# Performance work log

Measured on AMD Instinct MI355X. Metric: run time of the kernel, lower is better.

Reference implementation:

```python
import jax, jax.numpy as jnp
import numpy as np

WINDOW_SIZES = (8, 16)
NUM_HEADS = 4
EPS_LN = 1e-5
EPS_Z = 1e-6


def _unfold(x, ws, st):
    # torch nn.Unfold -> [B*L, ws*ws, C] with L blocks row-major over (nh, nw)
    B, C, H, W = x.shape
    nh = (H - ws) // st + 1
    nw = (W - ws) // st + 1
    ih = (jnp.arange(nh) * st)[:, None] + jnp.arange(ws)[None, :]  # [nh, ws]
    iw = (jnp.arange(nw) * st)[:, None] + jnp.arange(ws)[None, :]  # [nw, ws]
    p = x[:, :, ih][:, :, :, :, iw]            # [B,C,nh,ws,nw,ws]
    p = p.transpose(0, 2, 4, 3, 5, 1)          # [B,nh,nw,ws,ws,C]
    return p.reshape(B * nh * nw, ws * ws, C)


def _fold(win, ws, st, H, W):
    # torch nn.Fold: scatter-add overlapping patches back to [B,C,H,W]
    B_, N, C = win.shape
    nh = (H - ws) // st + 1
    nw = (W - ws) // st + 1
    B = B_ // (nh * nw)
    ih = (jnp.arange(nh) * st)[:, None] + jnp.arange(ws)[None, :]
    iw = (jnp.arange(nw) * st)[:, None] + jnp.arange(ws)[None, :]
    p = win.reshape(B, nh, nw, ws, ws, C).transpose(0, 5, 1, 3, 2, 4)  # [B,C,nh,ws,nw,ws]
    out = jnp.zeros((B, C, H, W), win.dtype)
    return out.at[:, :, ih[:, :, None, None], iw[None, None, :, :]].add(p)


def _ln(x, g, b):
    m = jnp.mean(x, -1, keepdims=True)
    v = jnp.var(x, -1, keepdims=True)
    return (x - m) * jax.lax.rsqrt(v + EPS_LN) * g + b


def _forward(high_stage, low_stage, conv_w, conv_b, ln_g, ln_b,
             wq, bq, wk, bk, wv, bv, wo, bo, window_weights, alpha):
    # 1x1 conv: high_channel -> base_channel
    hs = jnp.einsum('bchw,oc->bohw', high_stage, conv_w) + conv_b[None, :, None, None]
    B, C, Hl, Wl = low_stage.shape
    H, W = hs.shape[2], hs.shape[3]
    s = Hl // H                      # Scale_spatial
    h = NUM_HEADS
    dh = C // h
    folded = []
    for i, ws in enumerate(WINDOW_SIZES):
        wsq = s * ws
        # queries from low stage (overlapping scaled windows)
        qw = _ln(_unfold(low_stage, wsq, wsq // 2), ln_g, ln_b)   # [B_,Nq,C]
        B_, Nq, _ = qw.shape
        q = (qw @ wq.T + bq).reshape(B_, Nq, h, dh).transpose(0, 2, 1, 3)
        q = jax.nn.elu(q) + 1.0                                    # [B_,h,Nq,dh]
        # keys/values from high stage windows
        fw = _ln(_unfold(hs, ws, ws // 2), ln_g, ln_b)             # [B_,Nk,C]
        Nk = fw.shape[1]
        k = (fw @ wk.T + bk).reshape(B_, Nk, h, dh).transpose(0, 2, 1, 3)
        k = jax.nn.elu(k) + 1.0
        v = (fw @ wv.T + bv).reshape(B_, Nk, h, dh).transpose(0, 2, 1, 3)
        # kernelized linear attention
        kmean = jnp.mean(k, axis=2)                                # [B_,h,dh]
        z = 1.0 / (jnp.einsum('bhnd,bhd->bhn', q, kmean) + EPS_Z)[..., None]
        kv = jnp.einsum('bhnd,bhne->bhde', k, v) / ws              # (k^T/sqrt(ws)) @ (v/sqrt(ws))
        out = jnp.einsum('bhnd,bhde->bhne', q, kv) * z * window_weights[i]
        out = out.transpose(0, 2, 1, 3).reshape(B_, Nq, C) @ wo.T + bo
        folded.append(_fold(out, wsq, wsq // 2, Hl, Wl))
    out = sum(folded) / len(folded)
    final = alpha[0] * out + (1.0 - alpha[0]) * low_stage
    return out, final


def setup_inputs():
    key = jax.random.key(0)
    ks = jax.random.split(key, 8)
    B, Ch, Cb, Hh, Wh, s = 8, 256, 128, 64, 64, 2
    sc = 0.02
    d = {}
    d['high_stage'] = jax.random.normal(ks[0], (B, Ch, Hh, Wh), jnp.float32)
    d['low_stage'] = jax.random.normal(ks[1], (B, Cb, Hh * s, Wh * s), jnp.float32)
    d['conv_w'] = jax.random.normal(ks[2], (Cb, Ch), jnp.float32) * sc
    d['conv_b'] = jnp.zeros((Cb,), jnp.float32)
    d['ln_g'] = jnp.ones((Cb,), jnp.float32)
    d['ln_b'] = jnp.zeros((Cb,), jnp.float32)
    d['wq'] = jax.random.normal(ks[3], (Cb, Cb), jnp.float32) * sc
    d['bq'] = jnp.zeros((Cb,), jnp.float32)
    d['wk'] = jax.random.normal(ks[4], (Cb, Cb), jnp.float32) * sc
    d['bk'] = jnp.zeros((Cb,), jnp.float32)
    d['wv'] = jax.random.normal(ks[5], (Cb, Cb), jnp.float32) * sc
    d['bv'] = jnp.zeros((Cb,), jnp.float32)
    d['wo'] = jax.random.normal(ks[6], (Cb, Cb), jnp.float32) * sc
    d['bo'] = jnp.zeros((Cb,), jnp.float32)
    d['window_weights'] = jnp.ones((len(WINDOW_SIZES),), jnp.float32)
    d['alpha'] = jnp.ones((1,), jnp.float32)
    return d


def reference(high_stage, low_stage, conv_w, conv_b, ln_g, ln_b,
              wq, bq, wk, bk, wv, bv, wo, bo, window_weights, alpha):
    out, final = _forward(high_stage, low_stage, conv_w, conv_b, ln_g, ln_b,
                          wq, bq, wk, bk, wv, bv, wo, bo, window_weights, alpha)
    return (out, final)
```

## Files before the change

### kernel.cpp

```cpp
#include <hip/hip_runtime.h>

#define NB 8
#define CH 256
#define CB 128
#define HSW 64
#define HSP (HSW*HSW)
#define LW 128
#define LP (LW*LW)

typedef __attribute__((ext_vector_type(8))) short bf16x8;
typedef __attribute__((ext_vector_type(4))) float f32x4;

__device__ inline ushort f2bf(float x) {
  uint u = __float_as_uint(x);
  uint r = (u + 0x7fffu + ((u >> 16) & 1u)) >> 16;
  return (ushort)r;
}
__device__ inline float bf2f(uint u) { return __uint_as_float(u << 16); }

__device__ inline bf16x8 ldg8(const ushort* p) {
  uint2 lo = *(const uint2*)p;
  uint2 hi = *(const uint2*)(p + 4);
  uint4 u = make_uint4(lo.x, lo.y, hi.x, hi.y);
  return *(bf16x8*)&u;
}

static constexpr size_t S_KVU = (size_t)NB*HSP*CB;

static constexpr size_t OFF_KCM   = 0;
static constexpr size_t OFF_VCM   = OFF_KCM + S_KVU/2;
static constexpr size_t OFF_KM8   = OFF_VCM + S_KVU/2;
static constexpr size_t OFF_KV8T  = OFF_KM8 + (size_t)1800*128;
static constexpr size_t OFF_KM16  = OFF_KV8T + (size_t)1800*4096/2;
static constexpr size_t OFF_KV16T = OFF_KM16 + (size_t)392*128;
static constexpr size_t OFF_WQB   = OFF_KV16T + (size_t)392*4096/2;
static constexpr size_t OFF_WKB   = OFF_WQB + 8192;
static constexpr size_t OFF_WVB   = OFF_WKB + 8192;
static constexpr size_t OFF_WOB   = OFF_WVB + 8192;
static constexpr size_t OFF_CWB   = OFF_WOB + 8192;

__global__ __launch_bounds__(256)
void k_castw(const float* __restrict__ s0, const float* __restrict__ s1,
             const float* __restrict__ s2, const float* __restrict__ s3,
             const float* __restrict__ s4,
             ushort* __restrict__ d0, ushort* __restrict__ d1,
             ushort* __restrict__ d2, ushort* __restrict__ d3,
             ushort* __restrict__ d4) {
  int y = blockIdx.y;
  const float* s; ushort* d; int n;
  if (y == 0)      { s = s0; d = d0; n = 16384; }
  else if (y == 1) { s = s1; d = d1; n = 16384; }
  else if (y == 2) { s = s2; d = d2; n = 16384; }
  else if (y == 3) { s = s3; d = d3; n = 16384; }
  else             { s = s4; d = d4; n = 32768; }
  int i = (blockIdx.x * 256 + threadIdx.x) * 8;
  if (i >= n) return;
  float4 a = *(const float4*)(s + i);
  float4 b = *(const float4*)(s + i + 4);
  bf16x8 pk;
  pk[0]=(short)f2bf(a.x); pk[1]=(short)f2bf(a.y); pk[2]=(short)f2bf(a.z); pk[3]=(short)f2bf(a.w);
  pk[4]=(short)f2bf(b.x); pk[5]=(short)f2bf(b.y); pk[6]=(short)f2bf(b.z); pk[7]=(short)f2bf(b.w);
  *(bf16x8*)(d + i) = pk;
}

#define A1S 264
__global__ __launch_bounds__(256)
void k_convkv(const float* __restrict__ high, const ushort* __restrict__ cwb,
              const float* __restrict__ cb, const float* __restrict__ lng,
              const float* __restrict__ lnb,
              const ushort* __restrict__ wkb, const float* __restrict__ bk,
              const ushort* __restrict__ wvb, const float* __restrict__ bv,
              ushort* __restrict__ kcm, ushort* __restrict__ vcm) {
  __shared__ __align__(16) ushort As1[64*A1S];
  __shared__ __align__(16) ushort As2[64*136];
  __shared__ float red[512];
  __shared__ float stat_m[64], stat_r[64];
  int t = threadIdx.x;
  size_t pixbase = (size_t)blockIdx.x * 64;
  int b = blockIdx.x >> 6;
  int prel = (int)(pixbase & (HSP - 1));
  const float* xb = high + (size_t)b*CH*HSP + prel;

  {
    int p = t & 63;
    int cp = (t >> 6) * 2;
    #pragma unroll 4
    for (int pass = 0; pass < 32; ++pass) {
      int c = pass*8 + cp;
      float v0 = xb[(size_t)c*HSP + p];
      float v1 = xb[(size_t)(c+1)*HSP + p];
      uint pk = (uint)f2bf(v0) | ((uint)f2bf(v1) << 16);
      *(uint*)&As1[p*A1S + c] = pk;
    }
  }
  __syncthreads();

  int l = t & 63, h = t >> 6;
  int lr = l & 15, lg = l >> 4;
  int n0 = h * 32;

  f32x4 acc[4][2];
  #pragma unroll
  for (int mt = 0; mt < 4; ++mt)
    #pragma unroll
    for (int nt = 0; nt < 2; ++nt) acc[mt][nt] = (f32x4){0.f,0.f,0.f,0.f};
  #pragma unroll
  for (int k0 = 0; k0 < 256; k0 += 32) {
    bf16x8 a[4], bw[2];
    #pragma unroll
    for (int mt = 0; mt < 4; ++mt)
      a[mt] = *(bf16x8*)&As1[(mt*16+lr)*A1S + k0 + lg*8];
    #pragma unroll
    for (int nt = 0; nt < 2; ++nt)
      bw[nt] = *(const bf16x8*)(cwb + (size_t)(n0 + nt*16 + lr)*256 + k0 + lg*8);
    #pragma unroll
    for (int mt = 0; mt < 4; ++mt)
      #pragma unroll
      for (int nt = 0; nt < 2; ++nt)
        acc[mt][nt] = __builtin_amdgcn_mfma_f32_16x16x32_bf16(a[mt], bw[nt], acc[mt][nt], 0,0,0);
  }
  {
    float cb0 = cb[n0 + lr], cb1 = cb[n0 + 16 + lr];
    #pragma unroll
    for (int mt = 0; mt < 4; ++mt)
      #pragma unroll
      for (int r = 0; r < 4; ++r) { acc[mt][0][r] += cb0; acc[mt][1][r] += cb1; }
  }
  #pragma unroll
  for (int mt = 0; mt < 4; ++mt)
    #pragma unroll
    for (int r = 0; r < 4; ++r) {
      float a0 = acc[mt][0][r], a1 = acc[mt][1][r];
      float s = a0 + a1, ss = a0*a0 + a1*a1;
      #pragma unroll
      for (int off = 1; off < 16; off <<= 1) {
        s  += __shfl_xor(s, off, 64);
        ss += __shfl_xor(ss, off, 64);
      }
      if (lr == 0) {
        int p = mt*16 + lg*4 + r;
        red[h*64 + p] = s;
        red[256 + h*64 + p] = ss;
      }
    }
  __syncthreads();
  if (t < 64) {
    float s  = red[t] + red[64+t] + red[128+t] + red[192+t];
    float ss = red[256+t] + red[320+t] + red[384+t] + red[448+t];
    float m = s * (1.f/128.f);
    float var = ss * (1.f/128.f) - m*m;
    stat_m[t] = m;
    stat_r[t] = rsqrtf(fmaxf(var, 0.f) + 1e-5f);
  }
  __syncthreads();
  {
    float g0 = lng[n0+lr], b0 = lnb[n0+lr];
    float g1 = lng[n0+16+lr], b1 = lnb[n0+16+lr];
    #pragma unroll
    for (int mt = 0; mt < 4; ++mt)
      #pragma unroll
      for (int r = 0; r < 4; ++r) {
        int p = mt*16 + lg*4 + r;
        float m = stat_m[p], rr = stat_r[p];
        As2[p*136 + n0 + lr]      = f2bf((acc[mt][0][r] - m)*rr*g0 + b0);
        As2[p*136 + n0 + 16 + lr] = f2bf((acc[mt][1][r] - m)*rr*g1 + b1);
      }
  }
  __syncthreads();

  f32x4 ak[4][2], av[4][2];
  #pragma unroll
  for (int mt = 0; mt < 4; ++mt)
    #pragma unroll
    for (int nt = 0; nt < 2; ++nt) { ak[mt][nt] = (f32x4){0.f,0.f,0.f,0.f}; av[mt][nt] = (f32x4){0.f,0.f,0.f,0.f}; }
  #pragma unroll
  for (int k0 = 0; k0 < 128; k0 += 32) {
    bf16x8 a[4], bkf[2], bvf[2];
    #pragma unroll
    for (int mt = 0; mt < 4; ++mt)
      a[mt] = *(bf16x8*)&As2[(mt*16+lr)*136 + k0 + lg*8];
    #pragma unroll
    for (int nt = 0; nt < 2; ++nt) {
      bkf[nt] = *(const bf16x8*)(wkb + (size_t)(n0 + nt*16 + lr)*128 + k0 + lg*8);
      bvf[nt] = *(const bf16x8*)(wvb + (size_t)(n0 + nt*16 + lr)*128 + k0 + lg*8);
    }
    #pragma unroll
    for (int mt = 0; mt < 4; ++mt)
      #pragma unroll
      for (int nt = 0; nt < 2; ++nt) {
        ak[mt][nt] = __builtin_amdgcn_mfma_f32_16x16x32_bf16(a[mt], bkf[nt], ak[mt][nt], 0,0,0);
        av[mt][nt] = __builtin_amdgcn_mfma_f32_16x16x32_bf16(a[mt], bvf[nt], av[mt][nt], 0,0,0);
      }
  }
  __syncthreads();
  {
    float bk0 = bk[n0+lr], bk1 = bk[n0+16+lr];
    #pragma unroll
    for (int mt = 0; mt < 4; ++mt)
      #pragma unroll
      for (int r = 0; r < 4; ++r) {
        int p = mt*16 + lg*4 + r;
        float v0 = ak[mt][0][r] + bk0;
        float v1 = ak[mt][1][r] + bk1;
        v0 = (v0 > 0.f) ? v0 + 1.f : __expf(v0);
        v1 = (v1 > 0.f) ? v1 + 1.f : __expf(v1);
        As2[p*136 + n0 + lr]      = f2bf(v0);
        As2[p*136 + n0 + 16 + lr] = f2bf(v1);
      }
  }
  __syncthreads();
  #pragma unroll
  for (int pass = 0; pass < 4; ++pass) {
    int oct = t & 7;
    int c = (t >> 3) + pass*32;
    bf16x8 pk;
    #pragma unroll
    for (int i = 0; i < 8; ++i) pk[i] = (short)As2[(oct*8 + i)*136 + c];
    *(bf16x8*)(kcm + ((size_t)b*CB + c)*HSP + prel + oct*8) = pk;
  }
  __syncthreads();
  {
    float bv0 = bv[n0+lr], bv1 = bv[n0+16+lr];
    #pragma unroll
    for (int mt = 0; mt < 4; ++mt)
      #pragma unroll
      for (int r = 0; r < 4; ++r) {
        int p = mt*16 + lg*4 + r;
        As2[p*136 + n0 + lr]      = f2bf(av[mt][0][r] + bv0);
        As2[p*136 + n0 + 16 + lr] = f2bf(av[mt][1][r] + bv1);
      }
  }
  __syncthreads();
  #pragma unroll
  for (int pass = 0; pass < 4; ++pass) {
    int oct = t & 7;
    int c = (t >> 3) + pass*32;
    bf16x8 pk;
    #pragma unroll
    for (int i = 0; i < 8; ++i) pk[i] = (short)As2[(oct*8 + i)*136 + c];
    *(bf16x8*)(vcm + ((size_t)b*CB + c)*HSP + prel + oct*8) = pk;
  }
}

template<int WS>
__device__ __forceinline__ void win_do(const ushort* __restrict__ kb,
                                       const ushort* __restrict__ vb,
                                       int y0, int x0, int lr, int lg,
                                       float* __restrict__ kmp,
                                       ushort* __restrict__ kvp) {
  constexpr int KS = (WS*WS)/32;
  constexpr float kvscale = 1.f/WS;
  constexpr float kmscale = 1.f/(WS*WS);
  #pragma unroll
  for (int h = 0; h < 4; ++h) {
    f32x4 c00 = {0,0,0,0}, c01 = {0,0,0,0}, c10 = {0,0,0,0}, c11 = {0,0,0,0};
    float sm0 = 0.f, sm1 = 0.f;
    #pragma unroll
    for (int ks = 0; ks < KS; ++ks) {
      int kk = ks*32 + lg*8;
      int yy = kk / WS, xx = kk - (kk/WS)*WS;
      size_t off = (size_t)(y0+yy)*HSW + x0 + xx;
      const ushort* v0p = vb + (size_t)(h*32+lr)*HSP + off;
      const ushort* k0p = kb + (size_t)(h*32+lr)*HSP + off;
      bf16x8 a0 = ldg8(v0p);
      bf16x8 a1 = ldg8(v0p + (size_t)16*HSP);
      bf16x8 b0 = ldg8(k0p);
      bf16x8 b1 = ldg8(k0p + (size_t)16*HSP);
      c00 = __builtin_amdgcn_mfma_f32_16x16x32_bf16(a0, b0, c00, 0,0,0);
      c01 = __builtin_amdgcn_mfma_f32_16x16x32_bf16(a0, b1, c01, 0,0,0);
      c10 = __builtin_amdgcn_mfma_f32_16x16x32_bf16(a1, b0, c10, 0,0,0);
      c11 = __builtin_amdgcn_mfma_f32_16x16x32_bf16(a1, b1, c11, 0,0,0);
      #pragma unroll
      for (int j = 0; j < 8; ++j) {
        sm0 += bf2f((uint)(ushort)b0[j]);
        sm1 += bf2f((uint)(ushort)b1[j]);
      }
    }
    sm0 += __shfl_xor(sm0, 16, 64); sm0 += __shfl_xor(sm0, 32, 64);
    sm1 += __shfl_xor(sm1, 16, 64); sm1 += __shfl_xor(sm1, 32, 64);
    if (lg == 0) {
      kmp[h*32 + lr]      = sm0 * kmscale;
      kmp[h*32 + 16 + lr] = sm1 * kmscale;
    }
    ushort* kh = kvp + h*1024;
    #pragma unroll
    for (int r = 0; r < 4; ++r) {
      kh[(lg*4+r)*32 + lr]           = f2bf(c00[r]*kvscale);
      kh[(lg*4+r)*32 + 16 + lr]      = f2bf(c01[r]*kvscale);
      kh[(16+lg*4+r)*32 + lr]        = f2bf(c10[r]*kvscale);
      kh[(16+lg*4+r)*32 + 16 + lr]   = f2bf(c11[r]*kvscale);
    }
  }
}

__global__ __launch_bounds__(256)
void k_winmfma(const ushort* __restrict__ kcm, const ushort* __restrict__ vcm,
               float* __restrict__ km8, ushort* __restrict__ kv8T,
               float* __restrict__ km16, ushort* __restrict__ kv16T) {
  int t = threadIdx.x;
  int wv = t >> 6, l = t & 63;
  int lr = l & 15, lg = l >> 4;
  int gw = blockIdx.x*4 + wv;
  if (gw < 1800) {
    int b = gw / 225, rem = gw - b*225;
    int wi = rem / 15, wj = rem - (rem/15)*15;
    win_do<8>(kcm + (size_t)b*CB*HSP, vcm + (size_t)b*CB*HSP,
              wi*4, wj*4, lr, lg,
              km8 + (size_t)gw*128, kv8T + (size_t)gw*4096);
  } else {
    int w = gw - 1800;
    int b = w / 49, rem = w - b*49;
    int wi = rem / 7, wj = rem - (rem/7)*7;
    win_do<16>(kcm + (size_t)b*CB*HSP, vcm + (size_t)b*CB*HSP,
               wi*8, wj*8, lr, lg,
               km16 + (size_t)w*128, kv16T + (size_t)w*4096);
  }
}

__global__ __launch_bounds__(512)
void k_qfold(const float* __restrict__ low,
             const float* __restrict__ lng, const float* __restrict__ lnb,
             const ushort* __restrict__ wqb, const float* __restrict__ bq,
             const float* __restrict__ km8, const ushort* __restrict__ kv8T,
             const float* __restrict__ km16, const ushort* __restrict__ kv16T,
             const float* __restrict__ wwt,
             const ushort* __restrict__ wobf, const float* __restrict__ bo,
             const float* __restrict__ alpha,
             float* __restrict__ out0, float* __restrict__ out1) {
  __shared__ __align__(16) char smem_raw[128*136*2];
  ushort* As = (ushort*)smem_raw;
  float* Cs = (float*)smem_raw;
  float* redA = (float*)smem_raw;
  float* redB = redA + 2048;
  __shared__ float stat_m[128], stat_r[128];
  int t = threadIdx.x;
  int hx = t >> 8;
  int th = t & 255;
  int rbase = hx * 64;
  int bid = blockIdx.x;
  int swz = (bid & 7) * 128 + (bid >> 3);
  int bb = swz >> 7;
  int tile = swz & 127;
  int y0 = (tile >> 3) * 8;
  int x0t = (tile & 7) * 16;
  int x0 = x0t + hx * 8;

  int q  = t & 31;
  int cg = t >> 5;
  int row_q = q >> 2, xq = q & 3;
  float4 val[8];
  {
    const float* basep = low + ((size_t)bb*CB + cg*8)*LP + (size_t)(y0+row_q)*LW + x0t + xq*4;
    float s4[4] = {0.f,0.f,0.f,0.f}, ss4[4] = {0.f,0.f,0.f,0.f};
    #pragma unroll
    for (int j = 0; j < 8; ++j) {
      val[j] = *(const float4*)(basep + (size_t)j*LP);
      s4[0] += val[j].x; ss4[0] += val[j].x*val[j].x;
      s4[1] += val[j].y; ss4[1] += val[j].y*val[j].y;
      s4[2] += val[j].z; ss4[2] += val[j].z*val[j].z;
      s4[3] += val[j].w; ss4[3] += val[j].w*val[j].w;
    }
    #pragma unroll
    for (int i = 0; i < 4; ++i) {
      redA[cg*128 + q*4 + i] = s4[i];
      redB[cg*128 + q*4 + i] = ss4[i];
    }
  }
  __syncthreads();
  if (t < 128) {
    float s = 0.f, ss = 0.f;
    #pragma unroll
    for (int g = 0; g < 16; ++g) { s += redA[g*128 + t]; ss += redB[g*128 + t]; }
    float m = s * (1.f/128.f);
    float var = ss * (1.f/128.f) - m*m;
    stat_m[t] = m;
    stat_r[t] = rsqrtf(fmaxf(var, 0.f) + 1e-5f);
  }
  __syncthreads();
  {
    float g[8], bvls[8];
    #pragma unroll
    for (int j = 0; j < 8; ++j) { g[j] = lng[cg*8+j]; bvls[j] = lnb[cg*8+j]; }
    #pragma unroll
    for (int i = 0; i < 4; ++i) {
      int tp = q*4 + i;
      float m = stat_m[tp], r = stat_r[tp];
      float xv[8];
      #pragma unroll
      for (int j = 0; j < 8; ++j) {
        float xc = (i==0) ? val[j].x : (i==1) ? val[j].y : (i==2) ? val[j].z : val[j].w;
        xv[j] = xc;
      }
      bf16x8 pk;
      #pragma unroll
      for (int j = 0; j < 8; ++j)
        pk[j] = (short)f2bf((xv[j] - m)*r*g[j] + bvls[j]);
      int ar = (xq>>1)*64 + row_q*8 + (xq&1)*4 + i;
      *(bf16x8*)&As[ar*136 + cg*8] = pk;
    }
  }
  __syncthreads();

  int l = th & 63, h = th >> 6;
  int lr = l & 15, lg = l >> 4;
  int n0 = h * 32;

  f32x4 qa[4][2];
  #pragma unroll
  for (int mt = 0; mt < 4; ++mt)
    #pragma unroll
    for (int nt = 0; nt < 2; ++nt) qa[mt][nt] = (f32x4){0.f,0.f,0.f,0.f};
  #pragma unroll
  for (int k0 = 0; k0 < 128; k0 += 32) {
    bf16x8 a[4], bf[2];
    #pragma unroll
    for (int mt = 0; mt < 4; ++mt)
      a[mt] = *(bf16x8*)&As[(rbase + mt*16+lr)*136 + k0 + lg*8];
    #pragma unroll
    for (int nt = 0; nt < 2; ++nt)
      bf[nt] = *(const bf16x8*)(wqb + (size_t)(n0 + nt*16 + lr)*128 + k0 + lg*8);
    #pragma unroll
    for (int mt = 0; mt < 4; ++mt)
      #pragma unroll
      for (int nt = 0; nt < 2; ++nt)
        qa[mt][nt] = __builtin_amdgcn_mfma_f32_16x16x32_bf16(a[mt], bf[nt], qa[mt][nt], 0,0,0);
  }
  __syncthreads();
  {
    float b0 = bq[n0+lr], b1 = bq[n0+16+lr];
    #pragma unroll
    for (int mt = 0; mt < 4; ++mt)
      #pragma unroll
      for (int r = 0; r < 4; ++r) {
        int pp = mt*16 + lg*4 + r;
        float v0 = qa[mt][0][r] + b0;
        float v1 = qa[mt][1][r] + b1;
        v0 = (v0 > 0.f) ? v0 + 1.f : __expf(v0);
        v1 = (v1 > 0.f) ? v1 + 1.f : __expf(v1);
        As[(rbase+pp)*136 + n0 + lr]      = f2bf(v0);
        As[(rbase+pp)*136 + n0 + 16 + lr] = f2bf(v1);
      }
  }
  __syncthreads();

  bf16x8 aq[4];
  #pragma unroll
  for (int mt = 0; mt < 4; ++mt)
    aq[mt] = *(bf16x8*)&As[(rbase + mt*16+lr)*136 + h*32 + lg*8];

  float ww0 = wwt[0], ww1 = wwt[1];

  bf16x8 kmf = {0,0,0,0,0,0,0,0};
  {
    int s = lr;
    int wsi = (s >> 2) & 1;
    int n = wsi ? 7 : 15;
    int ar = (y0 >> (3+wsi)) - 1 + ((s>>1)&1);
    int ac = (x0 >> (3+wsi)) - 1 + (s&1);
    if (s < 8 && ar >= 0 && ar < n && ac >= 0 && ac < n) {
      size_t w = ((size_t)bb*n + ar)*n + ac;
      const float* kmp = (wsi ? km16 : km8) + w*(size_t)CB + h*32 + lg*8;
      #pragma unroll
      for (int j = 0; j < 8; ++j) kmf[j] = (short)f2bf(kmp[j]);
    }
  }
  f32x4 z4 = {0.f,0.f,0.f,0.f};
  f32x4 fm[4];
  #pragma unroll
  for (int mt = 0; mt < 4; ++mt) {
    f32x4 zf = __builtin_amdgcn_mfma_f32_16x16x32_bf16(aq[mt], kmf, z4, 0,0,0);
    float wwl = ((lr >> 2) & 1) ? ww1 : ww0;
    #pragma unroll
    for (int r = 0; r < 4; ++r) fm[mt][r] = wwl / (zf[r] + 1e-6f);
  }

  float acc0[4][4], acc1[4][4];
  #pragma unroll
  for (int mt = 0; mt < 4; ++mt)
    #pragma unroll
    for (int r = 0; r < 4; ++r) { acc0[mt][r] = 0.f; acc1[mt][r] = 0.f; }

  #pragma unroll
  for (int s = 0; s < 8; ++s) {
    const int wsi = s >> 2;
    const int n = wsi ? 7 : 15;
    int ar = (y0 >> (3+wsi)) - 1 + ((s>>1)&1);
    int ac = (x0 >> (3+wsi)) - 1 + (s&1);
    if (ar < 0 || ar >= n || ac < 0 || ac >= n) continue;
    size_t w = ((size_t)bb*n + ar)*n + ac;
    const ushort* kvp = (wsi ? kv16T : kv8T) + w*4096 + h*1024 + lg*8;
    bf16x8 b0 = *(const bf16x8*)(kvp + (size_t)lr*32);
    bf16x8 b1 = *(const bf16x8*)(kvp + (size_t)(16+lr)*32);
    #pragma unroll
    for (int mt = 0; mt < 4; ++mt) {
      f32x4 pv0 = __builtin_amdgcn_mfma_f32_16x16x32_bf16(aq[mt], b0, z4, 0,0,0);
      f32x4 pv1 = __builtin_amdgcn_mfma_f32_16x16x32_bf16(aq[mt], b1, z4, 0,0,0);
      #pragma unroll
      for (int r = 0; r < 4; ++r) {
        float fv = __shfl(fm[mt][r], (l & 48) | s, 64);
        acc0[mt][r] += fv * pv0[r];
        acc1[mt][r] += fv * pv1[r];
      }
    }
  }
  __syncthreads();
  #pragma unroll
  for (int mt = 0; mt < 4; ++mt)
    #pragma unroll
    for (int r = 0; r < 4; ++r) {
      int pp = mt*16 + lg*4 + r;
      As[(rbase+pp)*136 + n0 + lr]      = f2bf(acc0[mt][r]);
      As[(rbase+pp)*136 + n0 + 16 + lr] = f2bf(acc1[mt][r]);
    }
  __syncthreads();

  f32x4 oc[4][2];
  #pragma unroll
  for (int mt = 0; mt < 4; ++mt)
    #pragma unroll
    for (int nt = 0; nt < 2; ++nt) oc[mt][nt] = (f32x4){0.f,0.f,0.f,0.f};
  #pragma unroll
  for (int k0 = 0; k0 < 128; k0 += 32) {
    bf16x8 a[4], bf[2];
    #pragma unroll
    for (int mt = 0; mt < 4; ++mt)
      a[mt] = *(bf16x8*)&As[(rbase + mt*16+lr)*136 + k0 + lg*8];
    #pragma unroll
    for (int nt = 0; nt < 2; ++nt)
      bf[nt] = *(const bf16x8*)(wobf + (size_t)(n0 + nt*16 + lr)*128 + k0 + lg*8);
    #pragma unroll
    for (int mt = 0; mt < 4; ++mt)
      #pragma unroll
      for (int nt = 0; nt < 2; ++nt)
        oc[mt][nt] = __builtin_amdgcn_mfma_f32_16x16x32_bf16(a[mt], bf[nt], oc[mt][nt], 0,0,0);
  }

  float aB = alpha[0];
  int xg = t & 3;
  int row = (t >> 2) & 7;
  int oib = t >> 5;
  int xh = xg >> 1;
  int pxl = (xg & 1) * 4;
  int py_g = y0 + row;
  int cy8  = (py_g >= 8)  + (py_g <= 119);
  int cy16 = (py_g >= 16) + (py_g <= 111);
  float mult[4];
  #pragma unroll
  for (int i = 0; i < 4; ++i) {
    int px_g = x0t + xg*4 + i;
    int cx8  = (px_g >= 8)  + (px_g <= 119);
    int cx16 = (px_g >= 16) + (px_g <= 111);
    mult[i] = (float)(cy8*cx8 + cy16*cx16);
  }
  size_t rowaddr = (size_t)py_g*LW + x0t + xg*4;

  #pragma unroll
  for (int nt = 0; nt < 2; ++nt) {
    __syncthreads();
    {
      int oi = h*16 + lr;
      #pragma unroll
      for (int mt = 0; mt < 4; ++mt)
        *(f32x4*)&Cs[(rbase + oi)*68 + mt*16 + lg*4] = oc[mt][nt];
    }
    __syncthreads();
    #pragma unroll
    for (int pp = 0; pp < 4; ++pp) {
      int oi = oib + pp*16;
      int o = ((oi >> 4) << 5) + (nt << 4) + (oi & 15);
      float4 c4 = *(float4*)&Cs[(xh*64 + oi)*68 + row*8 + pxl];
      float bov = bo[o];
      size_t addr = ((size_t)bb*CB + o)*LP + rowaddr;
      float4 lw = *(const float4*)(low + addr);
      float g0 = 0.5f*(c4.x + bov*mult[0]);
      float g1 = 0.5f*(c4.y + bov*mult[1]);
      float g2 = 0.5f*(c4.z + bov*mult[2]);
      float g3 = 0.5f*(c4.w + bov*mult[3]);
      *(float4*)(out0 + addr) = make_float4(g0,g1,g2,g3);
      *(float4*)(out1 + addr) = make_float4(aB*g0 + (1.f-aB)*lw.x,
                                            aB*g1 + (1.f-aB)*lw.y,
                                            aB*g2 + (1.f-aB)*lw.z,
                                            aB*g3 + (1.f-aB)*lw.w);
    }
  }
}

extern "C" void kernel_launch(void* const* d_in, const int* in_sizes, int n_in,
                              void* d_out, int out_size, void* d_ws, size_t ws_size,
                              hipStream_t stream) {
  const float* high  = (const float*)d_in[0];
  const float* low   = (const float*)d_in[1];
  const float* cw    = (const float*)d_in[2];
  const float* cb    = (const float*)d_in[3];
  const float* lng   = (const float*)d_in[4];
  const float* lnb   = (const float*)d_in[5];
  const float* wq    = (const float*)d_in[6];
  const float* bq    = (const float*)d_in[7];
  const float* wk    = (const float*)d_in[8];
  const float* bk    = (const float*)d_in[9];
  const float* wv    = (const float*)d_in[10];
  const float* bv    = (const float*)d_in[11];
  const float* wo    = (const float*)d_in[12];
  const float* bo    = (const float*)d_in[13];
  const float* wwt   = (const float*)d_in[14];
  const float* alpha = (const float*)d_in[15];

  float* ws   = (float*)d_ws;
  ushort* kcm = (ushort*)(ws + OFF_KCM);
  ushort* vcm = (ushort*)(ws + OFF_VCM);
  float* km8  = ws + OFF_KM8;
  ushort* kv8T  = (ushort*)(ws + OFF_KV8T);
  float* km16 = ws + OFF_KM16;
  ushort* kv16T = (ushort*)(ws + OFF_KV16T);
  ushort* wqb = (ushort*)(ws + OFF_WQB);
  ushort* wkb = (ushort*)(ws + OFF_WKB);
  ushort* wvb = (ushort*)(ws + OFF_WVB);
  ushort* wob = (ushort*)(ws + OFF_WOB);
  ushort* cwb = (ushort*)(ws + OFF_CWB);

  float* out0 = (float*)d_out;
  float* out1 = out0 + (size_t)NB*CB*LP;

  k_castw<<<dim3(16,5), 256, 0, stream>>>(wq, wk, wv, wo, cw, wqb, wkb, wvb, wob, cwb);
  k_convkv<<<512, 256, 0, stream>>>(high, cwb, cb, lng, lnb, wkb, bk, wvb, bv, kcm, vcm);
  k_winmfma<<<548, 256, 0, stream>>>(kcm, vcm, km8, kv8T, km16, kv16T);
  k_qfold<<<1024, 512, 0, stream>>>(low, lng, lnb, wqb, bq, km8, kv8T, km16, kv16T,
                                    wwt, wob, bo, alpha, out0, out1);
}
```

Baseline: 140.5 us.

## Stage window row strips in LDS and share them across overlapping windows

Measured after the change: 112.9 us. -19.6%, faster.

```diff
diff --git a/kernel.cpp b/kernel.cpp
--- a/kernel.cpp
+++ b/kernel.cpp
@@ -242,78 +242,140 @@
   }
 }
 
-template<int WS>
-__device__ __forceinline__ void win_do(const ushort* __restrict__ kb,
-                                       const ushort* __restrict__ vb,
-                                       int y0, int x0, int lr, int lg,
-                                       float* __restrict__ kmp,
-                                       ushort* __restrict__ kvp) {
-  constexpr int KS = (WS*WS)/32;
-  constexpr float kvscale = 1.f/WS;
-  constexpr float kmscale = 1.f/(WS*WS);
-  #pragma unroll
-  for (int h = 0; h < 4; ++h) {
-    f32x4 c00 = {0,0,0,0}, c01 = {0,0,0,0}, c10 = {0,0,0,0}, c11 = {0,0,0,0};
-    float sm0 = 0.f, sm1 = 0.f;
-    #pragma unroll
-    for (int ks = 0; ks < KS; ++ks) {
-      int kk = ks*32 + lg*8;
-      int yy = kk / WS, xx = kk - (kk/WS)*WS;
-      size_t off = (size_t)(y0+yy)*HSW + x0 + xx;
-      const ushort* v0p = vb + (size_t)(h*32+lr)*HSP + off;
-      const ushort* k0p = kb + (size_t)(h*32+lr)*HSP + off;
-      bf16x8 a0 = ldg8(v0p);
-      bf16x8 a1 = ldg8(v0p + (size_t)16*HSP);
-      bf16x8 b0 = ldg8(k0p);
-      bf16x8 b1 = ldg8(k0p + (size_t)16*HSP);
-      c00 = __builtin_amdgcn_mfma_f32_16x16x32_bf16(a0, b0, c00, 0,0,0);
-      c01 = __builtin_amdgcn_mfma_f32_16x16x32_bf16(a0, b1, c01, 0,0,0);
-      c10 = __builtin_amdgcn_mfma_f32_16x16x32_bf16(a1, b0, c10, 0,0,0);
-      c11 = __builtin_amdgcn_mfma_f32_16x16x32_bf16(a1, b1, c11, 0,0,0);
-      #pragma unroll
-      for (int j = 0; j < 8; ++j) {
-        sm0 += bf2f((uint)(ushort)b0[j]);
-        sm1 += bf2f((uint)(ushort)b1[j]);
-      }
-    }
-    sm0 += __shfl_xor(sm0, 16, 64); sm0 += __shfl_xor(sm0, 32, 64);
-    sm1 += __shfl_xor(sm1, 16, 64); sm1 += __shfl_xor(sm1, 32, 64);
-    if (lg == 0) {
-      kmp[h*32 + lr]      = sm0 * kmscale;
-      kmp[h*32 + 16 + lr] = sm1 * kmscale;
-    }
-    ushort* kh = kvp + h*1024;
-    #pragma unroll
-    for (int r = 0; r < 4; ++r) {
-      kh[(lg*4+r)*32 + lr]           = f2bf(c00[r]*kvscale);
-      kh[(lg*4+r)*32 + 16 + lr]      = f2bf(c01[r]*kvscale);
-      kh[(16+lg*4+r)*32 + lr]        = f2bf(c10[r]*kvscale);
-      kh[(16+lg*4+r)*32 + 16 + lr]   = f2bf(c11[r]*kvscale);
-    }
-  }
-}
-
+#define WLDS 520
 __global__ __launch_bounds__(256)
-void k_winmfma(const ushort* __restrict__ kcm, const ushort* __restrict__ vcm,
-               float* __restrict__ km8, ushort* __restrict__ kv8T,
-               float* __restrict__ km16, ushort* __restrict__ kv16T) {
+void k_win2(const ushort* __restrict__ kcm, const ushort* __restrict__ vcm,
+            float* __restrict__ km8, ushort* __restrict__ kv8T,
+            float* __restrict__ km16, ushort* __restrict__ kv16T) {
+  __shared__ __align__(16) ushort kl[32*WLDS];
+  __shared__ __align__(16) ushort vl[32*WLDS];
   int t = threadIdx.x;
-  int wv = t >> 6, l = t & 63;
-  int lr = l & 15, lg = l >> 4;
-  int gw = blockIdx.x*4 + wv;
-  if (gw < 1800) {
-    int b = gw / 225, rem = gw - b*225;
-    int wi = rem / 15, wj = rem - (rem/15)*15;
-    win_do<8>(kcm + (size_t)b*CB*HSP, vcm + (size_t)b*CB*HSP,
-              wi*4, wj*4, lr, lg,
-              km8 + (size_t)gw*128, kv8T + (size_t)gw*4096);
+  int wv = t >> 6, l = t & 63, lr = l & 15, lg = l >> 4;
+  int blk = blockIdx.x;
+  if (blk < 480) {
+    int b = blk / 60, rem = blk - b*60;
+    int wi = rem >> 2, h = rem & 3;
+    const ushort* kb = kcm + ((size_t)b*CB + h*32)*HSP + wi*4*HSW;
+    const ushort* vb = vcm + ((size_t)b*CB + h*32)*HSP + wi*4*HSW;
+    #pragma unroll
+    for (int it = 0; it < 8; ++it) {
+      int e = it*256 + t;
+      int c = e >> 6, seg = e & 63;
+      *(uint4*)&kl[c*WLDS + seg*8] = *(const uint4*)(kb + (size_t)c*HSP + seg*8);
+      *(uint4*)&vl[c*WLDS + seg*8] = *(const uint4*)(vb + (size_t)c*HSP + seg*8);
+    }
+    __syncthreads();
+    for (int wj = wv; wj < 15; wj += 4) {
+      int x0 = wj*4;
+      f32x4 c00={0,0,0,0}, c01={0,0,0,0}, c10={0,0,0,0}, c11={0,0,0,0};
+      float sm0 = 0.f, sm1 = 0.f;
+      #pragma unroll
+      for (int ks = 0; ks < 2; ++ks) {
+        int kk = ks*32 + lg*8;
+        int yy = kk >> 3;
+        int lp = yy*HSW + x0;
+        bf16x8 a0 = ldg8(&vl[lr*WLDS + lp]);
+        bf16x8 a1 = ldg8(&vl[(16+lr)*WLDS + lp]);
+        bf16x8 b0 = ldg8(&kl[lr*WLDS + lp]);
+        bf16x8 b1 = ldg8(&kl[(16+lr)*WLDS + lp]);
+        c00 = __builtin_amdgcn_mfma_f32_16x16x32_bf16(a0, b0, c00, 0,0,0);
+        c01 = __builtin_amdgcn_mfma_f32_16x16x32_bf16(a0, b1, c01, 0,0,0);
+        c10 = __builtin_amdgcn_mfma_f32_16x16x32_bf16(a1, b0, c10, 0,0,0);
+        c11 = __builtin_amdgcn_mfma_f32_16x16x32_bf16(a1, b1, c11, 0,0,0);
+        #pragma unroll
+        for (int j = 0; j < 8; ++j) {
+          sm0 += bf2f((uint)(ushort)b0[j]);
+          sm1 += bf2f((uint)(ushort)b1[j]);
+        }
+      }
+      sm0 += __shfl_xor(sm0, 16, 64); sm0 += __shfl_xor(sm0, 32, 64);
+      sm1 += __shfl_xor(sm1, 16, 64); sm1 += __shfl_xor(sm1, 32, 64);
+      int gw = b*225 + wi*15 + wj;
+      if (lg == 0) {
+        km8[(size_t)gw*128 + h*32 + lr]      = sm0 * (1.f/64.f);
+        km8[(size_t)gw*128 + h*32 + 16 + lr] = sm1 * (1.f/64.f);
+      }
+      ushort* kh = kv8T + (size_t)gw*4096 + h*1024;
+      #pragma unroll
+      for (int r = 0; r < 4; ++r) {
+        kh[(lg*4+r)*32 + lr]         = f2bf(c00[r]*(1.f/8.f));
+        kh[(lg*4+r)*32 + 16 + lr]    = f2bf(c01[r]*(1.f/8.f));
+        kh[(16+lg*4+r)*32 + lr]      = f2bf(c10[r]*(1.f/8.f));
+        kh[(16+lg*4+r)*32 + 16 + lr] = f2bf(c11[r]*(1.f/8.f));
+      }
+    }
   } else {
-    int w = gw - 1800;
-    int b = w / 49, rem = w - b*49;
-    int wi = rem / 7, wj = rem - (rem/7)*7;
-    win_do<16>(kcm + (size_t)b*CB*HSP, vcm + (size_t)b*CB*HSP,
-               wi*8, wj*8, lr, lg,
-               km16 + (size_t)w*128, kv16T + (size_t)w*4096);
+    int bx = blk - 480;
+    int b = bx / 28, rem = bx - b*28;
+    int wi = rem >> 2, h = rem & 3;
+    int y0 = wi*8;
+    f32x4 d00[2], d01[2], d10[2], d11[2];
+    float s0[2], s1[2];
+    #pragma unroll
+    for (int w_ = 0; w_ < 2; ++w_) {
+      d00[w_] = (f32x4){0,0,0,0}; d01[w_] = (f32x4){0,0,0,0};
+      d10[w_] = (f32x4){0,0,0,0}; d11[w_] = (f32x4){0,0,0,0};
+      s0[w_] = 0.f; s1[w_] = 0.f;
+    }
+    for (int yh = 0; yh < 2; ++yh) {
+      if (yh) __syncthreads();
+      const ushort* kb = kcm + ((size_t)b*CB + h*32)*HSP + (size_t)(y0 + yh*8)*HSW;
+      const ushort* vb = vcm + ((size_t)b*CB + h*32)*HSP + (size_t)(y0 + yh*8)*HSW;
+      #pragma unroll
+      for (int it = 0; it < 8; ++it) {
+        int e = it*256 + t;
+        int c = e >> 6, seg = e & 63;
+        *(uint4*)&kl[c*WLDS + seg*8] = *(const uint4*)(kb + (size_t)c*HSP + seg*8);
+        *(uint4*)&vl[c*WLDS + seg*8] = *(const uint4*)(vb + (size_t)c*HSP + seg*8);
+      }
+      __syncthreads();
+      #pragma unroll
+      for (int w_ = 0; w_ < 2; ++w_) {
+        int wj = wv + w_*4;
+        if (wj >= 7) continue;
+        int x0 = wj*8;
+        #pragma unroll
+        for (int ks = 0; ks < 4; ++ks) {
+          int kk = ks*32 + lg*8;
+          int yy = kk >> 4, xx = kk & 15;
+          int lp = yy*HSW + x0 + xx;
+          bf16x8 a0 = ldg8(&vl[lr*WLDS + lp]);
+          bf16x8 a1 = ldg8(&vl[(16+lr)*WLDS + lp]);
+          bf16x8 b0 = ldg8(&kl[lr*WLDS + lp]);
+          bf16x8 b1 = ldg8(&kl[(16+lr)*WLDS + lp]);
+          d00[w_] = __builtin_amdgcn_mfma_f32_16x16x32_bf16(a0, b0, d00[w_], 0,0,0);
+          d01[w_] = __builtin_amdgcn_mfma_f32_16x16x32_bf16(a0, b1, d01[w_], 0,0,0);
+          d10[w_] = __builtin_amdgcn_mfma_f32_16x16x32_bf16(a1, b0, d10[w_], 0,0,0);
+          d11[w_] = __builtin_amdgcn_mfma_f32_16x16x32_bf16(a1, b1, d11[w_], 0,0,0);
+          #pragma unroll
+          for (int j = 0; j < 8; ++j) {
+            s0[w_] += bf2f((uint)(ushort)b0[j]);
+            s1[w_] += bf2f((uint)(ushort)b1[j]);
+          }
+        }
+      }
+    }
+    #pragma unroll
+    for (int w_ = 0; w_ < 2; ++w_) {
+      int wj = wv + w_*4;
+      if (wj >= 7) continue;
+      float sm0 = s0[w_], sm1 = s1[w_];
+      sm0 += __shfl_xor(sm0, 16, 64); sm0 += __shfl_xor(sm0, 32, 64);
+      sm1 += __shfl_xor(sm1, 16, 64); sm1 += __shfl_xor(sm1, 32, 64);
+      int w = b*49 + wi*7 + wj;
+      if (lg == 0) {
+        km16[(size_t)w*128 + h*32 + lr]      = sm0 * (1.f/256.f);
+        km16[(size_t)w*128 + h*32 + 16 + lr] = sm1 * (1.f/256.f);
+      }
+      ushort* kh = kv16T + (size_t)w*4096 + h*1024;
+      #pragma unroll
+      for (int r = 0; r < 4; ++r) {
+        kh[(lg*4+r)*32 + lr]         = f2bf(d00[w_][r]*(1.f/16.f));
+        kh[(lg*4+r)*32 + 16 + lr]    = f2bf(d01[w_][r]*(1.f/16.f));
+        kh[(16+lg*4+r)*32 + lr]      = f2bf(d10[w_][r]*(1.f/16.f));
+        kh[(16+lg*4+r)*32 + 16 + lr] = f2bf(d11[w_][r]*(1.f/16.f));
+      }
+    }
   }
 }
 
@@ -623,7 +685,7 @@
 
   k_castw<<<dim3(16,5), 256, 0, stream>>>(wq, wk, wv, wo, cw, wqb, wkb, wvb, wob, cwb);
   k_convkv<<<512, 256, 0, stream>>>(high, cwb, cb, lng, lnb, wkb, bk, wvb, bv, kcm, vcm);
-  k_winmfma<<<548, 256, 0, stream>>>(kcm, vcm, km8, kv8T, km16, kv16T);
+  k_win2<<<704, 256, 0, stream>>>(kcm, vcm, km8, kv8T, km16, kv16T);
   k_qfold<<<1024, 512, 0, stream>>>(low, lng, lnb, wqb, bq, km8, kv8T, km16, kv16T,
                                     wwt, wob, bo, alpha, out0, out1);
 }
```
